# Optimization experiments

Measured on AMD Instinct MI355X. Metric: run time of the kernel, lower is better.

Reference implementation:

```python
import jax, jax.numpy as jnp
import numpy as np

N = 524288
FEAT = 32
RES = 256
BOUNDS = 1.3

OFFSETS = np.array([[-1.0, 0.0], [-0.5, 0.0], [0.5, 0.0], [1.0, 0.0],
                    [0.0, -1.0], [0.0, -0.5], [0.0, 0.5], [0.0, 1.0],
                    [0.5, 0.5], [0.5, -0.5], [-0.5, 0.5], [-0.5, -0.5]],
                   dtype=np.float32)  # [12, 2]


def setup_inputs() -> dict:
    key = jax.random.key(0)
    k = jax.random.split(key, 7)
    pts = (jax.random.uniform(k[0], (N, 3), jnp.float32) * 2.0 - 1.0) * (BOUNDS * 0.9)
    timestamps = jax.random.uniform(k[1], (N,), jnp.float32)
    scales = jax.random.uniform(k[2], (N, 3), jnp.float32) * 0.05
    plane0 = jax.random.normal(k[3], (FEAT, RES, RES), jnp.float32) * 0.1
    plane1 = jax.random.normal(k[4], (FEAT, RES, RES), jnp.float32) * 0.1
    plane2 = jax.random.normal(k[5], (FEAT, RES, RES), jnp.float32) * 0.1
    aabb = jnp.array([[BOUNDS, BOUNDS, BOUNDS], [-BOUNDS, -BOUNDS, -BOUNDS]], jnp.float32)
    return {"pts": pts, "timestamps": timestamps, "scales": scales,
            "plane0": plane0, "plane1": plane1, "plane2": plane2, "aabb": aabb}


def _bilinear_sample(plane, xy):
    # plane: [C, H, W]; xy: [M, 2] normalized coords in [-1, 1] (x -> W, y -> H)
    C, H, W = plane.shape
    x = jnp.clip((xy[:, 0] + 1.0) * 0.5 * (W - 1), 0.0, W - 1)
    y = jnp.clip((xy[:, 1] + 1.0) * 0.5 * (H - 1), 0.0, H - 1)
    x0 = jnp.floor(x)
    y0 = jnp.floor(y)
    wx = x - x0
    wy = y - y0
    x0i = x0.astype(jnp.int32)
    y0i = y0.astype(jnp.int32)
    x1i = jnp.minimum(x0i + 1, W - 1)
    y1i = jnp.minimum(y0i + 1, H - 1)
    f00 = plane[:, y0i, x0i]  # [C, M]
    f10 = plane[:, y0i, x1i]
    f01 = plane[:, y1i, x0i]
    f11 = plane[:, y1i, x1i]
    out = (f00 * ((1.0 - wx) * (1.0 - wy)) + f10 * (wx * (1.0 - wy))
           + f01 * ((1.0 - wx) * wy) + f11 * (wx * wy))
    return out.T  # [M, C]


def _interpolate_mul(pts_n, scales, planes):
    offsets = jnp.asarray(OFFSETS)  # [12, 2]
    pairs = ((0, 1), (0, 2), (1, 2))
    interp = 1.0
    for i, (q, r) in enumerate(pairs):
        base = pts_n[:, (q, r)]                                   # [N, 2]
        so = scales[:, (q, r)][:, None, :] * offsets[None, :, :]  # [N, 12, 2]
        pts13 = jnp.concatenate([base[:, None, :], base[:, None, :] + so], axis=1)  # [N, 13, 2]
        feat = _bilinear_sample(planes[i], pts13.reshape(-1, 2))  # [N*13, C]
        feat = feat.reshape(-1, 13, feat.shape[-1]).mean(axis=1)  # [N, C]
        interp = interp * feat
    return interp


def reference(pts, timestamps, scales, plane0, plane1, plane2, aabb):
    # normalize_aabb: aabb = [[+b,+b,+b], [-b,-b,-b]]
    pts_n = (pts - aabb[0]) * (2.0 / (aabb[1] - aabb[0])) - 1.0
    pts_n = pts_n.reshape(-1, pts_n.shape[-1])
    del timestamps  # detached / unused in feature interpolation
    return _interpolate_mul(pts_n, scales, (plane0, plane1, plane2))
```

## Files before the change

### kernel.cpp

```cpp
#include <hip/hip_runtime.h>
#include <hip/hip_fp16.h>

#define RES 256
#define FEAT 32
#define PLANE_ELEMS (FEAT * RES * RES)
#define NBINS 32768
#define TQ_BLOCKS (3 * 256 * 4)

typedef unsigned u32x4 __attribute__((ext_vector_type(4)));


__device__ inline unsigned spread3(unsigned v) {
    unsigned r = 0;
    r |= (v & 1u);
    r |= (v & 2u) << 2;
    r |= (v & 4u) << 4;
    r |= (v & 8u) << 6;
    r |= (v & 16u) << 8;
    return r;
}

__global__ __launch_bounds__(256) void pre_tq_hist(const float* __restrict__ p0,
                                                   const float* __restrict__ p1,
                                                   const float* __restrict__ p2,
                                                   __half* __restrict__ outp,
                                                   const float* __restrict__ pts,
                                                   const float* __restrict__ aabb,
                                                   int* __restrict__ hist,
                                                   int* __restrict__ keys, int n) {
    int tid = threadIdx.x;
    if (blockIdx.x < TQ_BLOCKS) {
        __shared__ unsigned lds[64 * 17];
        int bid = blockIdx.x;
        int pl = bid >> 10;
        int rem = bid & 1023;
        int y = rem >> 2;
        int xbase = (rem & 3) * 64;
        const float* in = pl == 0 ? p0 : (pl == 1 ? p1 : p2);

        {
            int x = tid & 63;
            int c2b = (tid >> 6) * 4;
#pragma unroll
            for (int cc = 0; cc < 4; ++cc) {
                int c2 = c2b + cc;
                float f0 = in[(2 * c2) * (RES * RES) + y * RES + xbase + x];
                float f1 = in[(2 * c2 + 1) * (RES * RES) + y * RES + xbase + x];
                unsigned u = (unsigned)__half_as_ushort(__float2half(f0)) |
                             ((unsigned)__half_as_ushort(__float2half(f1)) << 16);
                lds[x * 17 + c2] = u;
            }
        }
        __syncthreads();

        {
            unsigned* o32 = reinterpret_cast<unsigned*>(outp) + (size_t)pl * (PLANE_ELEMS / 2);
            int c2 = tid & 15;
            int xo = (tid >> 4) & 15;
#pragma unroll
            for (int xx = 0; xx < 4; ++xx) {
                int x = xx * 16 + xo;
                o32[(size_t)(y * 256 + xbase + x) * 16 + c2] = lds[x * 17 + c2];
            }
        }
    } else {
        int i = (blockIdx.x - TQ_BLOCKS) * 256 + tid;
        if (i >= n) return;
        float a00 = aabb[0], a01 = aabb[1], a02 = aabb[2];
        float a10 = aabb[3], a11 = aabb[4], a12 = aabb[5];
        float px = (pts[i * 3 + 0] - a00) * (2.0f / (a10 - a00)) - 1.0f;
        float py = (pts[i * 3 + 1] - a01) * (2.0f / (a11 - a01)) - 1.0f;
        float pz = (pts[i * 3 + 2] - a02) * (2.0f / (a12 - a02)) - 1.0f;
        unsigned ux = (unsigned)min(max((int)((px + 1.0f) * 16.0f), 0), 31);
        unsigned uy = (unsigned)min(max((int)((py + 1.0f) * 16.0f), 0), 31);
        unsigned uz = (unsigned)min(max((int)((pz + 1.0f) * 16.0f), 0), 31);
        int key = (int)(spread3(ux) | (spread3(uy) << 1) | (spread3(uz) << 2));
        keys[i] = key;
        atomicAdd(&hist[key], 1);
    }
}

__global__ __launch_bounds__(1024) void scan_hist(int* __restrict__ hist) {
    __shared__ int sums[1024];
    int t = threadIdx.x;
    int base = t * 32;
    int4 L[8];
    const int4* h4 = reinterpret_cast<const int4*>(hist + base);
#pragma unroll
    for (int i = 0; i < 8; ++i) L[i] = h4[i];
    int s = 0;
#pragma unroll
    for (int i = 0; i < 8; ++i) s += L[i].x + L[i].y + L[i].z + L[i].w;
    sums[t] = s;
    __syncthreads();
    for (int off = 1; off < 1024; off <<= 1) {
        int v = 0;
        if (t >= off) v = sums[t - off];
        __syncthreads();
        if (t >= off) sums[t] += v;
        __syncthreads();
    }
    int excl = (t == 0) ? 0 : sums[t - 1];
    int4* o4 = reinterpret_cast<int4*>(hist + base);
#pragma unroll
    for (int i = 0; i < 8; ++i) {
        int4 v;
        v.x = excl; excl += L[i].x;
        v.y = excl; excl += L[i].y;
        v.z = excl; excl += L[i].z;
        v.w = excl; excl += L[i].w;
        o4[i] = v;
    }
}

__global__ __launch_bounds__(256) void scatter_pack(const float* __restrict__ pts,
                                                    const float* __restrict__ scales,
                                                    const float* __restrict__ aabb,
                                                    const int* __restrict__ keys,
                                                    int* __restrict__ hist,
                                                    float* __restrict__ ppk,
                                                    int* __restrict__ idx_s, int n) {
    int i = blockIdx.x * 256 + threadIdx.x;
    if (i >= n) return;
    float a00 = aabb[0], a01 = aabb[1], a02 = aabb[2];
    float a10 = aabb[3], a11 = aabb[4], a12 = aabb[5];
    float px = (pts[i * 3 + 0] - a00) * (2.0f / (a10 - a00)) - 1.0f;
    float py = (pts[i * 3 + 1] - a01) * (2.0f / (a11 - a01)) - 1.0f;
    float pz = (pts[i * 3 + 2] - a02) * (2.0f / (a12 - a02)) - 1.0f;
    int pos = atomicAdd(&hist[keys[i]], 1);
    float4* o = reinterpret_cast<float4*>(ppk) + (size_t)pos * 2;
    o[0] = make_float4((px + 1.0f) * 127.5f, (py + 1.0f) * 127.5f, (pz + 1.0f) * 127.5f, 0.0f);
    o[1] = make_float4(scales[i * 3 + 0] * 63.75f, scales[i * 3 + 1] * 63.75f,
                       scales[i * 3 + 2] * 63.75f, 0.0f);
    idx_s[pos] = i;
}


#define MIX2(f0, f1, d, w)                                                              \
    asm("v_fma_mix_f32 %0, %1, %2, %0 op_sel_hi:[1,0,0]" : "+v"(f0) : "v"(d), "v"(w)); \
    asm("v_fma_mix_f32 %0, %1, %2, %0 op_sel:[1,0,0] op_sel_hi:[1,0,0]" : "+v"(f1) : "v"(d), "v"(w))

__device__ __forceinline__ void mix8(float* fs, u32x4 v, float w) {
    MIX2(fs[0], fs[1], v[0], w);
    MIX2(fs[2], fs[3], v[1], w);
    MIX2(fs[4], fs[5], v[2], w);
    MIX2(fs[6], fs[7], v[3], w);
}

__global__ __launch_bounds__(256) void wpf_main4(const float* __restrict__ ppk,
                                                 const int* __restrict__ idx_s,
                                                 const __half* __restrict__ planes,
                                                 float* __restrict__ out, int n, int swizzle) {
    int b = blockIdx.x;
    if (swizzle) {
        int nb = gridDim.x;
        int chunk = nb >> 3;
        b = (b & 7) * chunk + (b >> 3);
    }
    int t = b * 256 + threadIdx.x;
    int pt = t >> 2;
    int cg = t & 3;
    if (pt >= n) return;

    float4 a  = reinterpret_cast<const float4*>(ppk)[(size_t)pt * 2];
    float4 hh = reinterpret_cast<const float4*>(ppk)[(size_t)pt * 2 + 1];
    int chan = cg * 16;

    const int SI[13] = {2, 0, 1, 3, 4, 2, 2, 2, 2, 3, 3, 1, 1};
    const int SJ[13] = {2, 2, 2, 2, 2, 0, 1, 3, 4, 3, 1, 3, 1};

    float interp[8];

#pragma unroll 1
    for (int pr = 0; pr < 3; ++pr) {
        const __half* pbase = planes + (size_t)pr * PLANE_ELEMS;
        float cx = (pr == 2) ? a.y : a.x;
        float cy = (pr == 0) ? a.y : a.z;
        float hx = (pr == 2) ? hh.y : hh.x;
        float hy = (pr == 0) ? hh.y : hh.z;

        float wx[5], wxc[5], wy[5], wyc[5];
        int colA[5], rowA[5];
#pragma unroll
        for (int k = 0; k < 5; ++k) {
            float x = fmaf((float)(k - 2), hx, cx);
            int xi = (int)x;
            wx[k] = x - (float)xi;
            wxc[k] = 1.0f - wx[k];
            colA[k] = xi * 64 + chan;
            float y = fmaf((float)(k - 2), hy, cy);
            int yi = (int)y;
            wy[k] = y - (float)yi;
            wyc[k] = 1.0f - wy[k];
            rowA[k] = yi * (RES * 64);
        }

        float fs[8];
#pragma unroll
        for (int c = 0; c < 8; ++c) fs[c] = 0.0f;

        u32x4 A0, A1, A2, A3, B0, B1, B2, B3;

#define ISSUE(d0, d1, d2, d3, m)                                                          \
    {                                                                                     \
        unsigned vo0_ = (unsigned)(rowA[SJ[m]] + colA[SI[m]]);                            \
        unsigned vo1_ = vo0_ + 16384u;                                                    \
        asm volatile("global_load_dwordx4 %0, %1, %2"           : "=v"(d0) : "v"(vo0_), "s"(pbase)); \
        asm volatile("global_load_dwordx4 %0, %1, %2 offset:64" : "=v"(d1) : "v"(vo0_), "s"(pbase)); \
        asm volatile("global_load_dwordx4 %0, %1, %2"           : "=v"(d2) : "v"(vo1_), "s"(pbase)); \
        asm volatile("global_load_dwordx4 %0, %1, %2 offset:64" : "=v"(d3) : "v"(vo1_), "s"(pbase)); \
    }
#define WAIT4(b0, b1, b2, b3) \
    asm volatile("s_waitcnt vmcnt(4)" : "+v"(b0), "+v"(b1), "+v"(b2), "+v"(b3))
#define WAITZ(b0, b1, b2, b3) \
    asm volatile("s_waitcnt vmcnt(0)" : "+v"(b0), "+v"(b1), "+v"(b2), "+v"(b3))
#define CONSUME(m, b0, b1, b2, b3)                       \
    {                                                    \
        const int i_ = SI[m], j_ = SJ[m];                \
        float w00 = wxc[i_] * wyc[j_];                   \
        float w10 = wx[i_] * wyc[j_];                    \
        float w01 = wxc[i_] * wy[j_];                    \
        float w11 = wx[i_] * wy[j_];                     \
        mix8(fs, b0, w00);                               \
        mix8(fs, b1, w10);                               \
        mix8(fs, b2, w01);                               \
        mix8(fs, b3, w11);                               \
    }
#define STEP(s, C0, C1, C2, C3, N0, N1, N2, N3)  \
    ISSUE(N0, N1, N2, N3, (s) + 1);              \
    WAIT4(C0, C1, C2, C3);                       \
    CONSUME(s, C0, C1, C2, C3);

        ISSUE(A0, A1, A2, A3, 0);
        STEP(0,  A0, A1, A2, A3, B0, B1, B2, B3)
        STEP(1,  B0, B1, B2, B3, A0, A1, A2, A3)
        STEP(2,  A0, A1, A2, A3, B0, B1, B2, B3)
        STEP(3,  B0, B1, B2, B3, A0, A1, A2, A3)
        STEP(4,  A0, A1, A2, A3, B0, B1, B2, B3)
        STEP(5,  B0, B1, B2, B3, A0, A1, A2, A3)
        STEP(6,  A0, A1, A2, A3, B0, B1, B2, B3)
        STEP(7,  B0, B1, B2, B3, A0, A1, A2, A3)
        STEP(8,  A0, A1, A2, A3, B0, B1, B2, B3)
        STEP(9,  B0, B1, B2, B3, A0, A1, A2, A3)
        STEP(10, A0, A1, A2, A3, B0, B1, B2, B3)
        STEP(11, B0, B1, B2, B3, A0, A1, A2, A3)
        WAITZ(A0, A1, A2, A3);
        CONSUME(12, A0, A1, A2, A3);

#undef ISSUE
#undef WAIT4
#undef WAITZ
#undef CONSUME
#undef STEP

        if (pr == 0) {
#pragma unroll
            for (int c = 0; c < 8; ++c) interp[c] = fs[c];
        } else {
#pragma unroll
            for (int c = 0; c < 8; ++c) interp[c] *= fs[c];
        }
    }

    const float inv = 1.0f / 2197.0f;
    int oi = idx_s[pt];
    float4* o = reinterpret_cast<float4*>(out + (size_t)oi * 32 + cg * 8);
    o[0] = make_float4(interp[0] * inv, interp[1] * inv, interp[2] * inv, interp[3] * inv);
    o[1] = make_float4(interp[4] * inv, interp[5] * inv, interp[6] * inv, interp[7] * inv);
}

__global__ __launch_bounds__(256) void wpf_plain(const float* __restrict__ pts,
                                                 const float* __restrict__ scales,
                                                 const float* __restrict__ p0,
                                                 const float* __restrict__ p1,
                                                 const float* __restrict__ p2,
                                                 const float* __restrict__ aabb,
                                                 float* __restrict__ out, int n) {
    const float offx[13] = {0.f, -1.f, -0.5f, 0.5f, 1.f, 0.f, 0.f, 0.f, 0.f, 0.5f, 0.5f, -0.5f, -0.5f};
    const float offy[13] = {0.f, 0.f, 0.f, 0.f, 0.f, -1.f, -0.5f, 0.5f, 1.f, 0.5f, -0.5f, 0.5f, -0.5f};
    int t = blockIdx.x * 256 + threadIdx.x;
    int pt = t >> 3;
    int cg = t & 7;
    if (pt >= n) return;
    float a00 = aabb[0], a01 = aabb[1], a02 = aabb[2];
    float a10 = aabb[3], a11 = aabb[4], a12 = aabb[5];
    float px = (pts[pt * 3 + 0] - a00) * (2.0f / (a10 - a00)) - 1.0f;
    float py = (pts[pt * 3 + 1] - a01) * (2.0f / (a11 - a01)) - 1.0f;
    float pz = (pts[pt * 3 + 2] - a02) * (2.0f / (a12 - a02)) - 1.0f;
    float scx = scales[pt * 3 + 0], scy = scales[pt * 3 + 1], scz = scales[pt * 3 + 2];
    float4 interp = make_float4(1.f, 1.f, 1.f, 1.f);
    for (int pair = 0; pair < 3; ++pair) {
        const float* plane = pair == 0 ? p0 : (pair == 1 ? p1 : p2);
        float bx = pair == 2 ? py : px;
        float by = pair == 0 ? py : pz;
        float sx = pair == 2 ? scy : scx;
        float sy = pair == 0 ? scy : scz;
        float4 featsum = make_float4(0.f, 0.f, 0.f, 0.f);
        for (int s = 0; s < 13; ++s) {
            float x = fminf(fmaxf((bx + sx * offx[s] + 1.0f) * 127.5f, 0.0f), 255.0f);
            float y = fminf(fmaxf((by + sy * offy[s] + 1.0f) * 127.5f, 0.0f), 255.0f);
            float x0f = floorf(x), y0f = floorf(y);
            float wx = x - x0f, wy = y - y0f;
            int x0 = (int)x0f, y0 = (int)y0f;
            int x1 = min(x0 + 1, RES - 1), y1 = min(y0 + 1, RES - 1);
            float w00 = (1.0f - wx) * (1.0f - wy), w10 = wx * (1.0f - wy);
            float w01 = (1.0f - wx) * wy, w11 = wx * wy;
            int c0 = cg << 2;
            for (int c = 0; c < 4; ++c) {
                const float* pl = plane + (size_t)(c0 + c) * (RES * RES);
                float f = pl[y0 * RES + x0] * w00 + pl[y0 * RES + x1] * w10 +
                          pl[y1 * RES + x0] * w01 + pl[y1 * RES + x1] * w11;
                (&featsum.x)[c] += f;
            }
        }
        const float inv13 = 1.0f / 13.0f;
        interp.x *= featsum.x * inv13;
        interp.y *= featsum.y * inv13;
        interp.z *= featsum.z * inv13;
        interp.w *= featsum.w * inv13;
    }
    reinterpret_cast<float4*>(out)[(size_t)pt * 8 + cg] = interp;
}

extern "C" void kernel_launch(void* const* d_in, const int* in_sizes, int n_in,
                              void* d_out, int out_size, void* d_ws, size_t ws_size,
                              hipStream_t stream) {
    const float* pts    = (const float*)d_in[0];
    const float* scales = (const float*)d_in[2];
    const float* p0     = (const float*)d_in[3];
    const float* p1     = (const float*)d_in[4];
    const float* p2     = (const float*)d_in[5];
    const float* aabb   = (const float*)d_in[6];
    float* out = (float*)d_out;

    int n = in_sizes[0] / 3;
    int pt_blocks = (n + 255) / 256;

    size_t planes_hbytes = (size_t)3 * PLANE_ELEMS * sizeof(__half);
    size_t ppk_bytes = (size_t)n * 8 * sizeof(float);
    size_t idx_bytes = (size_t)n * sizeof(int);
    size_t key_bytes = (size_t)n * sizeof(int);
    size_t hist_bytes = (size_t)NBINS * sizeof(int);
    size_t need = planes_hbytes + ppk_bytes + idx_bytes + key_bytes + hist_bytes;

    if (ws_size >= need) {
        __half* planes_h = (__half*)d_ws;
        float*  ppk   = (float*)((char*)d_ws + planes_hbytes);
        int*    idx_s = (int*)((char*)ppk + ppk_bytes);
        int*    keys  = idx_s + n;
        int*    hist  = keys + n;

        hipMemsetAsync(hist, 0, hist_bytes, stream);
        pre_tq_hist<<<TQ_BLOCKS + pt_blocks, 256, 0, stream>>>(p0, p1, p2, planes_h,
                                                               pts, aabb, hist, keys, n);
        scan_hist<<<1, 1024, 0, stream>>>(hist);
        scatter_pack<<<pt_blocks, 256, 0, stream>>>(pts, scales, aabb, keys, hist,
                                                    ppk, idx_s, n);
        int main_blocks = (n * 4 + 255) / 256;
        int swizzle = (main_blocks % 8 == 0) ? 1 : 0;
        wpf_main4<<<main_blocks, 256, 0, stream>>>(ppk, idx_s, planes_h, out, n, swizzle);
    } else {
        int main_blocks = (n * 8 + 255) / 256;
        wpf_plain<<<main_blocks, 256, 0, stream>>>(pts, scales, p0, p1, p2, aabb, out, n);
    }
}
```

Measured before the change: 331.9 us.

## Unroll plane loop into continuous triple-buffered gather pipeline across all planes

Replaces the per-plane loop with one fully unrolled sequence of 39 gather steps that cross plane boundaries without draining the load queue. It moves from double to triple buffering, keeping two steps of loads in flight (vmcnt(8)), and computes the next plane's coordinates and weights while the previous plane's loads are still pending. The intent is to hide memory latency at the plane transitions and deepen overlap between gathers and arithmetic. In exchange it uses more vector registers, which could lower occupancy, and makes the code longer.

```diff
diff --git a/kernel.cpp b/kernel.cpp
--- a/kernel.cpp
+++ b/kernel.cpp
@@ -4,6 +4,7 @@
 #define RES 256
 #define FEAT 32
 #define PLANE_ELEMS (FEAT * RES * RES)
+#define PLANE_BYTES (PLANE_ELEMS * 2)
 #define NBINS 32768
 #define TQ_BLOCKS (3 * 256 * 4)
 
@@ -169,104 +170,120 @@
     const int SI[13] = {2, 0, 1, 3, 4, 2, 2, 2, 2, 3, 3, 1, 1};
     const int SJ[13] = {2, 2, 2, 2, 2, 0, 1, 3, 4, 3, 1, 3, 1};
 
+    float wx[2][5], wy[2][5];
+    int   cA[2][5], rA[2][5];
+    float fs[8] = {0, 0, 0, 0, 0, 0, 0, 0};
     float interp[8];
-
-#pragma unroll 1
-    for (int pr = 0; pr < 3; ++pr) {
-        const __half* pbase = planes + (size_t)pr * PLANE_ELEMS;
-        float cx = (pr == 2) ? a.y : a.x;
-        float cy = (pr == 0) ? a.y : a.z;
-        float hx = (pr == 2) ? hh.y : hh.x;
-        float hy = (pr == 0) ? hh.y : hh.z;
-
-        float wx[5], wxc[5], wy[5], wyc[5];
-        int colA[5], rowA[5];
-#pragma unroll
-        for (int k = 0; k < 5; ++k) {
-            float x = fmaf((float)(k - 2), hx, cx);
-            int xi = (int)x;
-            wx[k] = x - (float)xi;
-            wxc[k] = 1.0f - wx[k];
-            colA[k] = xi * 64 + chan;
-            float y = fmaf((float)(k - 2), hy, cy);
-            int yi = (int)y;
-            wy[k] = y - (float)yi;
-            wyc[k] = 1.0f - wy[k];
-            rowA[k] = yi * (RES * 64);
-        }
-
-        float fs[8];
-#pragma unroll
-        for (int c = 0; c < 8; ++c) fs[c] = 0.0f;
-
-        u32x4 A0, A1, A2, A3, B0, B1, B2, B3;
-
-#define ISSUE(d0, d1, d2, d3, m)                                                          \
+    u32x4 X0, X1, X2, X3, Y0, Y1, Y2, Y3, Z0, Z1, Z2, Z3;
+
+#define SETUP(SET, CX, CY, HX, HY, POFF)                 \
+    _Pragma("unroll")                                    \
+    for (int k = 0; k < 5; ++k) {                        \
+        float x_ = fmaf((float)(k - 2), (HX), (CX));     \
+        int xi_ = (int)x_;               \
+        wx[SET][k] = x_ - (float)xi_;                    \
+        cA[SET][k] = xi_ * 64 + chan;                    \
+        float y_ = fmaf((float)(k - 2), (HY), (CY));     \
+        int yi_ = (int)y_;                               \
+        wy[SET][k] = y_ - (float)yi_;                    \
+        rA[SET][k] = yi_ * (RES * 64) + (POFF);          \
+    }
+
+#define ISSUE(d0, d1, d2, d3, SET, M)                                                     \
     {                                                                                     \
-        unsigned vo0_ = (unsigned)(rowA[SJ[m]] + colA[SI[m]]);                            \
+        unsigned vo0_ = (unsigned)(rA[SET][SJ[M]] + cA[SET][SI[M]]);                      \
         unsigned vo1_ = vo0_ + 16384u;                                                    \
-        asm volatile("global_load_dwordx4 %0, %1, %2"           : "=v"(d0) : "v"(vo0_), "s"(pbase)); \
-        asm volatile("global_load_dwordx4 %0, %1, %2 offset:64" : "=v"(d1) : "v"(vo0_), "s"(pbase)); \
-        asm volatile("global_load_dwordx4 %0, %1, %2"           : "=v"(d2) : "v"(vo1_), "s"(pbase)); \
-        asm volatile("global_load_dwordx4 %0, %1, %2 offset:64" : "=v"(d3) : "v"(vo1_), "s"(pbase)); \
-    }
+        asm volatile("global_load_dwordx4 %0, %1, %2"           : "=v"(d0) : "v"(vo0_), "s"(planes)); \
+        asm volatile("global_load_dwordx4 %0, %1, %2 offset:64" : "=v"(d1) : "v"(vo0_), "s"(planes)); \
+        asm volatile("global_load_dwordx4 %0, %1, %2"           : "=v"(d2) : "v"(vo1_), "s"(planes)); \
+        asm volatile("global_load_dwordx4 %0, %1, %2 offset:64" : "=v"(d3) : "v"(vo1_), "s"(planes)); \
+    }
+#define WAIT8(b0, b1, b2, b3) \
+    asm volatile("s_waitcnt vmcnt(8)" : "+v"(b0), "+v"(b1), "+v"(b2), "+v"(b3))
 #define WAIT4(b0, b1, b2, b3) \
     asm volatile("s_waitcnt vmcnt(4)" : "+v"(b0), "+v"(b1), "+v"(b2), "+v"(b3))
 #define WAITZ(b0, b1, b2, b3) \
     asm volatile("s_waitcnt vmcnt(0)" : "+v"(b0), "+v"(b1), "+v"(b2), "+v"(b3))
-#define CONSUME(m, b0, b1, b2, b3)                       \
+#define CONSUME(SET, M, b0, b1, b2, b3)                  \
     {                                                    \
-        const int i_ = SI[m], j_ = SJ[m];                \
-        float w00 = wxc[i_] * wyc[j_];                   \
-        float w10 = wx[i_] * wyc[j_];                    \
-        float w01 = wxc[i_] * wy[j_];                    \
-        float w11 = wx[i_] * wy[j_];                     \
-        mix8(fs, b0, w00);                               \
-        mix8(fs, b1, w10);                               \
-        mix8(fs, b2, w01);                               \
-        mix8(fs, b3, w11);                               \
-    }
-#define STEP(s, C0, C1, C2, C3, N0, N1, N2, N3)  \
-    ISSUE(N0, N1, N2, N3, (s) + 1);              \
-    WAIT4(C0, C1, C2, C3);                       \
-    CONSUME(s, C0, C1, C2, C3);
-
-        ISSUE(A0, A1, A2, A3, 0);
-        STEP(0,  A0, A1, A2, A3, B0, B1, B2, B3)
-        STEP(1,  B0, B1, B2, B3, A0, A1, A2, A3)
-        STEP(2,  A0, A1, A2, A3, B0, B1, B2, B3)
-        STEP(3,  B0, B1, B2, B3, A0, A1, A2, A3)
-        STEP(4,  A0, A1, A2, A3, B0, B1, B2, B3)
-        STEP(5,  B0, B1, B2, B3, A0, A1, A2, A3)
-        STEP(6,  A0, A1, A2, A3, B0, B1, B2, B3)
-        STEP(7,  B0, B1, B2, B3, A0, A1, A2, A3)
-        STEP(8,  A0, A1, A2, A3, B0, B1, B2, B3)
-        STEP(9,  B0, B1, B2, B3, A0, A1, A2, A3)
-        STEP(10, A0, A1, A2, A3, B0, B1, B2, B3)
-        STEP(11, B0, B1, B2, B3, A0, A1, A2, A3)
-        WAITZ(A0, A1, A2, A3);
-        CONSUME(12, A0, A1, A2, A3);
-
+        float wxi = wx[SET][SI[M]], wyj = wy[SET][SJ[M]];\
+        float wxc = 1.0f - wxi, wyc = 1.0f - wyj;        \
+        mix8(fs, b0, wxc * wyc);                         \
+        mix8(fs, b1, wxi * wyc);                         \
+        mix8(fs, b2, wxc * wyj);                         \
+        mix8(fs, b3, wxi * wyj);                         \
+    }
+#define STEP(CS, CSET, ISET, C0, C1, C2, C3, N0, N1, N2, N3) \
+    ISSUE(N0, N1, N2, N3, ISET, ((CS) + 2) % 13);            \
+    WAIT8(C0, C1, C2, C3);                                   \
+    CONSUME(CSET, (CS) % 13, C0, C1, C2, C3);
+
+        SETUP(0, a.x, a.y, hh.x, hh.y, 0)
+        ISSUE(X0, X1, X2, X3, 0, 0);
+        ISSUE(Y0, Y1, Y2, Y3, 0, 1);
+        STEP(0,  0, 0, X0, X1, X2, X3, Z0, Z1, Z2, Z3)
+        STEP(1,  0, 0, Y0, Y1, Y2, Y3, X0, X1, X2, X3)
+        STEP(2,  0, 0, Z0, Z1, Z2, Z3, Y0, Y1, Y2, Y3)
+        STEP(3,  0, 0, X0, X1, X2, X3, Z0, Z1, Z2, Z3)
+        STEP(4,  0, 0, Y0, Y1, Y2, Y3, X0, X1, X2, X3)
+        STEP(5,  0, 0, Z0, Z1, Z2, Z3, Y0, Y1, Y2, Y3)
+        STEP(6,  0, 0, X0, X1, X2, X3, Z0, Z1, Z2, Z3)
+        STEP(7,  0, 0, Y0, Y1, Y2, Y3, X0, X1, X2, X3)
+        STEP(8,  0, 0, Z0, Z1, Z2, Z3, Y0, Y1, Y2, Y3)
+        STEP(9,  0, 0, X0, X1, X2, X3, Z0, Z1, Z2, Z3)
+        STEP(10, 0, 0, Y0, Y1, Y2, Y3, X0, X1, X2, X3)
+        SETUP(1, a.x, a.z, hh.x, hh.z, PLANE_BYTES)
+        STEP(11, 0, 1, Z0, Z1, Z2, Z3, Y0, Y1, Y2, Y3)
+        STEP(12, 0, 1, X0, X1, X2, X3, Z0, Z1, Z2, Z3)
+#pragma unroll
+        for (int c = 0; c < 8; ++c) { interp[c] = fs[c]; fs[c] = 0.0f; }
+        STEP(13, 1, 1, Y0, Y1, Y2, Y3, X0, X1, X2, X3)
+        STEP(14, 1, 1, Z0, Z1, Z2, Z3, Y0, Y1, Y2, Y3)
+        STEP(15, 1, 1, X0, X1, X2, X3, Z0, Z1, Z2, Z3)
+        STEP(16, 1, 1, Y0, Y1, Y2, Y3, X0, X1, X2, X3)
+        STEP(17, 1, 1, Z0, Z1, Z2, Z3, Y0, Y1, Y2, Y3)
+        STEP(18, 1, 1, X0, X1, X2, X3, Z0, Z1, Z2, Z3)
+        STEP(19, 1, 1, Y0, Y1, Y2, Y3, X0, X1, X2, X3)
+        STEP(20, 1, 1, Z0, Z1, Z2, Z3, Y0, Y1, Y2, Y3)
+        STEP(21, 1, 1, X0, X1, X2, X3, Z0, Z1, Z2, Z3)
+        STEP(22, 1, 1, Y0, Y1, Y2, Y3, X0, X1, X2, X3)
+        STEP(23, 1, 1, Z0, Z1, Z2, Z3, Y0, Y1, Y2, Y3)
+        SETUP(0, a.y, a.z, hh.y, hh.z, 2 * PLANE_BYTES)
+        STEP(24, 1, 0, X0, X1, X2, X3, Z0, Z1, Z2, Z3)
+        STEP(25, 1, 0, Y0, Y1, Y2, Y3, X0, X1, X2, X3)
+#pragma unroll
+        for (int c = 0; c < 8; ++c) { interp[c] *= fs[c]; fs[c] = 0.0f; }
+        STEP(26, 0, 0, Z0, Z1, Z2, Z3, Y0, Y1, Y2, Y3)
+        STEP(27, 0, 0, X0, X1, X2, X3, Z0, Z1, Z2, Z3)
+        STEP(28, 0, 0, Y0, Y1, Y2, Y3, X0, X1, X2, X3)
+        STEP(29, 0, 0, Z0, Z1, Z2, Z3, Y0, Y1, Y2, Y3)
+        STEP(30, 0, 0, X0, X1, X2, X3, Z0, Z1, Z2, Z3)
+        STEP(31, 0, 0, Y0, Y1, Y2, Y3, X0, X1, X2, X3)
+        STEP(32, 0, 0, Z0, Z1, Z2, Z3, Y0, Y1, Y2, Y3)
+        STEP(33, 0, 0, X0, X1, X2, X3, Z0, Z1, Z2, Z3)
+        STEP(34, 0, 0, Y0, Y1, Y2, Y3, X0, X1, X2, X3)
+        STEP(35, 0, 0, Z0, Z1, Z2, Z3, Y0, Y1, Y2, Y3)
+        STEP(36, 0, 0, X0, X1, X2, X3, Z0, Z1, Z2, Z3)
+        WAIT4(Y0, Y1, Y2, Y3);
+        CONSUME(0, 11, Y0, Y1, Y2, Y3);
+        WAITZ(Z0, Z1, Z2, Z3);
+        CONSUME(0, 12, Z0, Z1, Z2, Z3);
+
+#undef SETUP
 #undef ISSUE
+#undef WAIT8
 #undef WAIT4
 #undef WAITZ
 #undef CONSUME
 #undef STEP
 
-        if (pr == 0) {
-#pragma unroll
-            for (int c = 0; c < 8; ++c) interp[c] = fs[c];
-        } else {
-#pragma unroll
-            for (int c = 0; c < 8; ++c) interp[c] *= fs[c];
-        }
-    }
-
     const float inv = 1.0f / 2197.0f;
     int oi = idx_s[pt];
     float4* o = reinterpret_cast<float4*>(out + (size_t)oi * 32 + cg * 8);
-    o[0] = make_float4(interp[0] * inv, interp[1] * inv, interp[2] * inv, interp[3] * inv);
-    o[1] = make_float4(interp[4] * inv, interp[5] * inv, interp[6] * inv, interp[7] * inv);
+    o[0] = make_float4(interp[0] * fs[0] * inv, interp[1] * fs[1] * inv,
+                       interp[2] * fs[2] * inv, interp[3] * fs[3] * inv);
+    o[1] = make_float4(interp[4] * fs[4] * inv, interp[5] * fs[5] * inv,
+                       interp[6] * fs[6] * inv, interp[7] * fs[7] * inv);
 }
 
 __global__ __launch_bounds__(256) void wpf_plain(const float* __restrict__ pts,
```

Result: faster. 318.6 us (-4.0%).
